# Kernel tuning notes

Hardware: AMD Instinct MI355X
Metric: run time of the kernel (lower is better)

The kernel has to match this reference:

```python
import jax, jax.numpy as jnp
import numpy as np

# Initial EMA thresholds (module init args T_feature, T_weight)
T_FEATURE = 3.0
T_WEIGHT = 0.3
EMA = 0.95  # update: T = 0.95*T + 0.05*absmax
STRIDE, PADDING, DILATION = 1, 1, 1


def setup_inputs() -> dict:
    key = jax.random.key(0)
    k1, k2, k3 = jax.random.split(key, 3)
    x = jax.random.normal(k1, (8, 64, 28, 28), jnp.float32)
    weight = jax.random.normal(k2, (64, 64, 3, 3), jnp.float32) * 0.05
    bias = jax.random.normal(k3, (64,), jnp.float32) * 0.01
    # 256x256 LUT of (approximate) signed int8 products, indexed by q+128.
    # Here: exact product table (the common ApproxTorch baseline LUT).
    idx = jnp.arange(-128, 128, dtype=jnp.float32)
    lut = jnp.outer(idx, idx)
    return {"x": x, "weight": weight, "bias": bias, "lut": lut}


def _quant(v, scale):
    # symmetric int8 quantization with clipping threshold T => scale = T/127
    return jnp.clip(jnp.round(v / scale), -128, 127)


def _lut_conv(x, weight, bias, lut, T_f, T_w):
    s_x = T_f / 127.0
    s_w = T_w / 127.0
    Cout, Cin, K, _ = weight.shape
    # im2col patches: [B, Cin*K*K, OH, OW], feature dim ordered (Cin, Kh, Kw)
    patches = jax.lax.conv_general_dilated_patches(
        x, (K, K), (STRIDE, STRIDE), [(PADDING, PADDING)] * 2,
        rhs_dilation=(DILATION, DILATION))
    B, R, OH, OW = patches.shape
    qp = _quant(patches, s_x).astype(jnp.int32)
    qp = qp.reshape(B, R, OH * OW).transpose(0, 2, 1)  # [B, P, R]
    qw = _quant(weight.reshape(Cout, R), s_w).astype(jnp.int32)  # [Cout, R]

    def per_image(qpb):  # qpb: [P, R]
        # LUT-multiplied products summed over the receptive field
        vals = lut[qpb[:, None, :] + 128, qw[None, :, :] + 128]  # [P, Cout, R]
        return vals.sum(-1)  # [P, Cout]

    acc = jax.lax.map(per_image, qp)  # [B, P, Cout]
    out = acc.transpose(0, 2, 1).reshape(B, Cout, OH, OW)
    return out * (s_x * s_w) + bias[None, :, None, None]


def reference(x, weight, bias, lut):
    # EMA threshold update happens before the conv (update_T=True)
    T_f = EMA * T_FEATURE + (1.0 - EMA) * jnp.max(jnp.abs(x))
    T_w = EMA * T_WEIGHT + (1.0 - EMA) * jnp.max(jnp.abs(weight))
    return _lut_conv(x, weight, bias, lut, T_f, T_w)
```

## Files before the change

kernel.cpp:

```cpp
#include <hip/hip_runtime.h>
#include <stdint.h>

constexpr int Bn  = 8;
constexpr int Cc  = 64;
constexpr int Hh  = 28;
constexpr int Wd  = 28;
constexpr int NX  = Bn * Cc * Hh * Wd;
constexpr int NW  = 64 * 64 * 9;
constexpr int HW  = Hh * Wd;
constexpr int CHW = Cc * HW;

#if __has_builtin(__builtin_amdgcn_sdot4)
__device__ __forceinline__ int dot4(int a, int b, int c) {
  return __builtin_amdgcn_sdot4(a, b, c, false);
}
#else
__device__ __forceinline__ int dot4(int a, int b, int c) {
  return c + (int)(int8_t)(a)       * (int)(int8_t)(b)
           + (int)(int8_t)(a >> 8)  * (int)(int8_t)(b >> 8)
           + (int)(int8_t)(a >> 16) * (int)(int8_t)(b >> 16)
           + (a >> 24)              * (b >> 24);
}
#endif

__device__ __forceinline__ int q8i(float v, float s) {
  float q = rintf(v / s);
  q = fminf(fmaxf(q, -128.0f), 127.0f);
  return (int)q;
}

__global__ __launch_bounds__(256) void k_max(const float* __restrict__ x,
                                             const float* __restrict__ w,
                                             float* __restrict__ partial) {
  int bid = blockIdx.x, tid = threadIdx.x;
  const float4* src; int n4, nb, b0;
  if (bid < 64) { src = (const float4*)x; n4 = NX / 4; nb = 64; b0 = bid; }
  else          { src = (const float4*)w; n4 = NW / 4; nb = 32; b0 = bid - 64; }
  float m = 0.0f;
  for (int i = b0 * 256 + tid; i < n4; i += nb * 256) {
    float4 v = src[i];
    m = fmaxf(m, fmaxf(fmaxf(fabsf(v.x), fabsf(v.y)), fmaxf(fabsf(v.z), fabsf(v.w))));
  }
  for (int off = 32; off > 0; off >>= 1)
    m = fmaxf(m, __shfl_down(m, off));
  __shared__ float sm[4];
  if ((tid & 63) == 0) sm[tid >> 6] = m;
  __syncthreads();
  if (tid == 0) partial[bid] = fmaxf(fmaxf(sm[0], sm[1]), fmaxf(sm[2], sm[3]));
}

__global__ __launch_bounds__(256) void k_conv_fused(const float* __restrict__ x,
                                                    const float* __restrict__ w,
                                                    const float* __restrict__ partial,
                                                    const float* __restrict__ bias,
                                                    float* __restrict__ out) {
  __shared__ int   swd[9216];
  __shared__ int   sx[16 * 96];
  __shared__ float smax[8];
  __shared__ float s_scal[3];

  int bx = blockIdx.x, t = threadIdx.x;
  int wv = t >> 6;
  int oh = bx % 28;
  int b  = bx / 28;

  {
    float p  = (t < 96) ? partial[t] : 0.0f;
    float vx = (t < 64) ? p : 0.0f;
    float vw = (t >= 64 && t < 96) ? p : 0.0f;
    #pragma unroll
    for (int off = 32; off > 0; off >>= 1) {
      vx = fmaxf(vx, __shfl_down(vx, off));
      vw = fmaxf(vw, __shfl_down(vw, off));
    }
    if ((t & 63) == 0) { smax[wv] = vx; smax[4 + wv] = vw; }
    __syncthreads();
    if (t == 0) {
      float mxg = fmaxf(fmaxf(smax[0], smax[1]), fmaxf(smax[2], smax[3]));
      float mwg = fmaxf(fmaxf(smax[4], smax[5]), fmaxf(smax[6], smax[7]));
      float Tf = (float)(0.95 * 3.0) + (float)(1.0 - 0.95) * mxg;
      float Tw = (float)(0.95 * 0.3) + (float)(1.0 - 0.95) * mwg;
      float sxv = Tf / 127.0f, swv = Tw / 127.0f;
      s_scal[0] = sxv; s_scal[1] = swv; s_scal[2] = sxv * swv;
    }
    __syncthreads();
  }
  float s_x  = s_scal[0];
  float s_w  = s_scal[1];
  float s_xw = s_scal[2];

  #pragma unroll 4
  for (int k = 0; k < 36; ++k) {
    int u   = t + k * 256;
    int ci4 = u & 15;
    int kw  = (u >> 4) % 3;
    int kh  = (u / 48) % 3;
    int co  = u / 144;
    const float* ps = w + co * 576 + (ci4 * 4) * 9 + kh * 3 + kw;
    swd[u] = (q8i(ps[0],  s_w) & 255)
           | ((q8i(ps[9],  s_w) & 255) << 8)
           | ((q8i(ps[18], s_w) & 255) << 16)
           | ((q8i(ps[27], s_w) & 255) << 24);
  }

  for (int j = t; j < 1344; j += 256) {
    int r   = j / 448;
    int j2  = j - r * 448;
    int ci4 = j2 / 28;
    int iw  = j2 - ci4 * 28;
    int ih  = oh + r - 1;
    int v = 0;
    if (ih >= 0 && ih < Hh) {
      const float* ps = x + b * CHW + (ci4 * 4) * HW + ih * Wd + iw;
      v = (q8i(ps[0 * HW], s_x) & 255)
        | ((q8i(ps[1 * HW], s_x) & 255) << 8)
        | ((q8i(ps[2 * HW], s_x) & 255) << 16)
        | ((q8i(ps[3 * HW], s_x) & 255) << 24);
    }
    sx[ci4 * 96 + r * 32 + (iw + 1)] = v;
  }
  if (t < 192) {
    int ci4 = t / 12;
    int rs  = t - ci4 * 12;
    int r   = rs >> 2;
    int s   = rs & 3;
    int slot = (s == 0) ? 0 : (28 + s);
    sx[ci4 * 96 + r * 32 + slot] = 0;
  }
  __syncthreads();

  int ow = t & 31;
  int g  = t >> 5;
  int ow_r = (ow < 28) ? ow : 27;

  int acc[8];
  #pragma unroll
  for (int i = 0; i < 8; ++i) acc[i] = 0;

  const int4* w4p = (const int4*)swd;
  #pragma unroll
  for (int r = 0; r < 3; ++r) {
    #pragma unroll
    for (int kw = 0; kw < 3; ++kw) {
      int tap  = r * 3 + kw;
      int slot = ow_r + kw;
      #pragma unroll
      for (int c16 = 0; c16 < 4; ++c16) {
        int x0 = sx[(c16 * 4 + 0) * 96 + r * 32 + slot];
        int x1 = sx[(c16 * 4 + 1) * 96 + r * 32 + slot];
        int x2 = sx[(c16 * 4 + 2) * 96 + r * 32 + slot];
        int x3 = sx[(c16 * 4 + 3) * 96 + r * 32 + slot];
        #pragma unroll
        for (int coi = 0; coi < 8; ++coi) {
          int4 wvv = w4p[(g * 8 + coi) * 36 + tap * 4 + c16];
          int a = acc[coi];
          a = dot4(x0, wvv.x, a);
          a = dot4(x1, wvv.y, a);
          a = dot4(x2, wvv.z, a);
          a = dot4(x3, wvv.w, a);
          acc[coi] = a;
        }
      }
    }
  }

  if (ow < 28) {
    #pragma unroll
    for (int coi = 0; coi < 8; ++coi) {
      int co = g * 8 + coi;
      out[b * CHW + co * HW + oh * Wd + ow] = (float)acc[coi] * s_xw + bias[co];
    }
  }
}

extern "C" void kernel_launch(void* const* d_in, const int* in_sizes, int n_in,
                              void* d_out, int out_size, void* d_ws, size_t ws_size,
                              hipStream_t stream) {
  const float* x    = (const float*)d_in[0];
  const float* w    = (const float*)d_in[1];
  const float* bias = (const float*)d_in[2];
  float* out = (float*)d_out;
  float* partial = (float*)d_ws;

  k_max<<<96, 256, 0, stream>>>(x, w, partial);
  k_conv_fused<<<Bn * Hh, 256, 0, stream>>>(x, w, partial, bias, out);
}
```

Measured before the change: 86.66 us.

## Fuse absmax reduction into conv kernel with per-block redundant reduction

Removes the separate absmax kernel and workspace. Every conv block now scans all of x and the weights itself to compute the EMA thresholds. This drops one kernel launch and the inter-kernel dependency, but multiplies global/L2 read traffic by the number of blocks and adds a long serial loop before the conv work.

```diff
diff --git a/kernel.cpp b/kernel.cpp
--- a/kernel.cpp
+++ b/kernel.cpp
@@ -29,31 +29,10 @@
   return (int)q;
 }
 
-__global__ __launch_bounds__(256) void k_max(const float* __restrict__ x,
+__global__ __launch_bounds__(256) void k_all(const float* __restrict__ x,
                                              const float* __restrict__ w,
-                                             float* __restrict__ partial) {
-  int bid = blockIdx.x, tid = threadIdx.x;
-  const float4* src; int n4, nb, b0;
-  if (bid < 64) { src = (const float4*)x; n4 = NX / 4; nb = 64; b0 = bid; }
-  else          { src = (const float4*)w; n4 = NW / 4; nb = 32; b0 = bid - 64; }
-  float m = 0.0f;
-  for (int i = b0 * 256 + tid; i < n4; i += nb * 256) {
-    float4 v = src[i];
-    m = fmaxf(m, fmaxf(fmaxf(fabsf(v.x), fabsf(v.y)), fmaxf(fabsf(v.z), fabsf(v.w))));
-  }
-  for (int off = 32; off > 0; off >>= 1)
-    m = fmaxf(m, __shfl_down(m, off));
-  __shared__ float sm[4];
-  if ((tid & 63) == 0) sm[tid >> 6] = m;
-  __syncthreads();
-  if (tid == 0) partial[bid] = fmaxf(fmaxf(sm[0], sm[1]), fmaxf(sm[2], sm[3]));
-}
-
-__global__ __launch_bounds__(256) void k_conv_fused(const float* __restrict__ x,
-                                                    const float* __restrict__ w,
-                                                    const float* __restrict__ partial,
-                                                    const float* __restrict__ bias,
-                                                    float* __restrict__ out) {
+                                             const float* __restrict__ bias,
+                                             float* __restrict__ out) {
   __shared__ int   swd[9216];
   __shared__ int   sx[16 * 96];
   __shared__ float smax[8];
@@ -65,15 +44,25 @@
   int b  = bx / 28;
 
   {
-    float p  = (t < 96) ? partial[t] : 0.0f;
-    float vx = (t < 64) ? p : 0.0f;
-    float vw = (t >= 64 && t < 96) ? p : 0.0f;
+    float mx = 0.0f, mw = 0.0f;
+    const float4* x4 = (const float4*)x;
+    #pragma unroll 8
+    for (int i = t; i < NX / 4; i += 256) {
+      float4 v = x4[i];
+      mx = fmaxf(mx, fmaxf(fmaxf(fabsf(v.x), fabsf(v.y)), fmaxf(fabsf(v.z), fabsf(v.w))));
+    }
+    const float4* w4 = (const float4*)w;
+    #pragma unroll 4
+    for (int i = t; i < NW / 4; i += 256) {
+      float4 v = w4[i];
+      mw = fmaxf(mw, fmaxf(fmaxf(fabsf(v.x), fabsf(v.y)), fmaxf(fabsf(v.z), fabsf(v.w))));
+    }
     #pragma unroll
     for (int off = 32; off > 0; off >>= 1) {
-      vx = fmaxf(vx, __shfl_down(vx, off));
-      vw = fmaxf(vw, __shfl_down(vw, off));
+      mx = fmaxf(mx, __shfl_down(mx, off));
+      mw = fmaxf(mw, __shfl_down(mw, off));
     }
-    if ((t & 63) == 0) { smax[wv] = vx; smax[4 + wv] = vw; }
+    if ((t & 63) == 0) { smax[wv] = mx; smax[4 + wv] = mw; }
     __syncthreads();
     if (t == 0) {
       float mxg = fmaxf(fmaxf(smax[0], smax[1]), fmaxf(smax[2], smax[3]));
@@ -180,8 +169,6 @@
   const float* w    = (const float*)d_in[1];
   const float* bias = (const float*)d_in[2];
   float* out = (float*)d_out;
-  float* partial = (float*)d_ws;
 
-  k_max<<<96, 256, 0, stream>>>(x, w, partial);
-  k_conv_fused<<<Bn * Hh, 256, 0, stream>>>(x, w, partial, bias, out);
+  k_all<<<Bn * Hh, 256, 0, stream>>>(x, w, bias, out);
 }
```

Measured after the change: 153.3 us. 76.9% more time.
